# Optimization experiments

Hardware: AMD Instinct MI355X
Metric: run time of the kernel (lower is better)

The kernel has to match this reference:

```python
import jax, jax.numpy as jnp
from jax import lax
import numpy as np

B, T, IN, H, OUT = 1024, 512, 64, 128, 2
BN_EPS = 1e-5


def _gru_layer(x, w_ih, w_hh, b_ih, b_hh):
    # x: [B, T, F]; w_ih: [3H, F]; w_hh: [3H, H]; gate order = (r, z, n) as in PyTorch
    Bb = x.shape[0]
    Hh = w_hh.shape[1]
    xg = jnp.einsum('btf,gf->btg', x, w_ih) + b_ih  # precompute input gates [B, T, 3H]

    def step(h, xg_t):
        hg = h @ w_hh.T + b_hh                       # [B, 3H]
        xr, xz, xn = jnp.split(xg_t, 3, axis=-1)
        hr, hz, hn = jnp.split(hg, 3, axis=-1)
        r = jax.nn.sigmoid(xr + hr)
        z = jax.nn.sigmoid(xz + hz)
        n = jnp.tanh(xn + r * hn)
        h_new = (1.0 - z) * n + z * h
        return h_new, h_new

    h0 = jnp.zeros((Bb, Hh), dtype=x.dtype)
    _, ys = lax.scan(step, h0, jnp.swapaxes(xg, 0, 1))  # scan over time
    return jnp.swapaxes(ys, 0, 1)                        # [B, T, H]


def setup_inputs() -> dict:
    key = jax.random.key(0)
    ks = jax.random.split(key, 16)
    s_in = 1.0 / np.sqrt(H)  # PyTorch GRU init scale
    d = {
        'x': jax.random.normal(ks[0], (B, T, IN), dtype=jnp.float32),
        'w_ih0': jax.random.uniform(ks[1], (3 * H, IN), minval=-s_in, maxval=s_in),
        'w_hh0': jax.random.uniform(ks[2], (3 * H, H), minval=-s_in, maxval=s_in),
        'b_ih0': jax.random.uniform(ks[3], (3 * H,), minval=-s_in, maxval=s_in),
        'b_hh0': jax.random.uniform(ks[4], (3 * H,), minval=-s_in, maxval=s_in),
        'w_ih1': jax.random.uniform(ks[5], (3 * H, H), minval=-s_in, maxval=s_in),
        'w_hh1': jax.random.uniform(ks[6], (3 * H, H), minval=-s_in, maxval=s_in),
        'b_ih1': jax.random.uniform(ks[7], (3 * H,), minval=-s_in, maxval=s_in),
        'b_hh1': jax.random.uniform(ks[8], (3 * H,), minval=-s_in, maxval=s_in),
        'fc1_w': jax.random.normal(ks[9], (H // 2, H)) * 0.05,
        'fc1_b': jnp.zeros((H // 2,)),
        'fc2_w': jax.random.normal(ks[10], (OUT, H // 2)) * 0.05,
        'fc2_b': jnp.zeros((OUT,)),
        'bn_gamma': jnp.ones((H // 2,)),
        'bn_beta': jnp.zeros((H // 2,)),
        'bn_mean': jnp.zeros((H // 2,)),
        'bn_var': jnp.ones((H // 2,)),
    }
    return d


def reference(x, w_ih0, w_hh0, b_ih0, b_hh0, w_ih1, w_hh1, b_ih1, b_hh1,
              fc1_w, fc1_b, fc2_w, fc2_b, bn_gamma, bn_beta, bn_mean, bn_var):
    h1 = _gru_layer(x, w_ih0, w_hh0, b_ih0, b_hh0)   # [B, T, H]
    h2 = _gru_layer(h1, w_ih1, w_hh1, b_ih1, b_hh1)  # [B, T, H]
    out = h2[:, -1, :]                                # last timestep [B, H]
    # dropout = identity (eval mode)
    out = jax.nn.relu(out @ fc1_w.T + fc1_b)          # [B, H/2]
    out = (out - bn_mean) * jax.lax.rsqrt(bn_var + BN_EPS) * bn_gamma + bn_beta
    out = out @ fc2_w.T + fc2_b                       # [B, 2]
    return out
```

## Files before the change

### kernel.cpp

```cpp
#include <hip/hip_runtime.h>
#include <hip/hip_bf16.h>

namespace {

typedef _Float16 h16;
typedef _Float16 f16x8 __attribute__((ext_vector_type(8)));
typedef _Float16 f16x4 __attribute__((ext_vector_type(4)));
typedef _Float16 f16x2 __attribute__((ext_vector_type(2)));
typedef float    f32x4 __attribute__((ext_vector_type(4)));

constexpr int T_SEQ = 512;
constexpr int B_SZ  = 1024;
constexpr int H_DIM = 128;
constexpr int ROWS  = 16;
constexpr int NT    = 512;

template <int INDIM, typename InT, bool STORE_ALL>
__global__ __launch_bounds__(NT, 1)
void gru_mfma(const InT* __restrict__ in,
              const float* __restrict__ w_ih,
              const float* __restrict__ w_hh,
              const float* __restrict__ b_ih,
              const float* __restrict__ b_hh,
              h16*  __restrict__ h1out,
              float* __restrict__ h2out)
{
  constexpr int KSH  = H_DIM / 32;
  constexpr int KSX  = INDIM / 32;
  constexpr int KTOT = H_DIM + INDIM;
  constexpr int ROWP = KTOT + 8;

  __shared__ __align__(16) h16 hx[2][ROWS][ROWP];

  const int tid = threadIdx.x;
  const int wv  = tid >> 6;
  const int ln  = tid & 63;
  const int q   = ln >> 4;
  const int lr  = ln & 15;
  const int r0  = blockIdx.x * ROWS;
  const int j0  = wv * 16 + q * 4;

  f16x8 wA[3][KSH];
  f16x8 wB[3][KSX];
  #pragma unroll
  for (int p = 0; p < 3; ++p) {
    const int g = p * H_DIM + wv * 16 + lr;
    #pragma unroll
    for (int ks = 0; ks < KSH; ++ks) {
      const float* pw = w_hh + (size_t)g * H_DIM + ks * 32 + q * 8;
      const float4 v0 = *(const float4*)(pw);
      const float4 v1 = *(const float4*)(pw + 4);
      f16x8 f;
      f[0]=(h16)v0.x; f[1]=(h16)v0.y; f[2]=(h16)v0.z; f[3]=(h16)v0.w;
      f[4]=(h16)v1.x; f[5]=(h16)v1.y; f[6]=(h16)v1.z; f[7]=(h16)v1.w;
      wA[p][ks] = f;
    }
    #pragma unroll
    for (int ks = 0; ks < KSX; ++ks) {
      const float* pw = w_ih + (size_t)g * INDIM + ks * 32 + q * 8;
      const float4 v0 = *(const float4*)(pw);
      const float4 v1 = *(const float4*)(pw + 4);
      f16x8 f;
      f[0]=(h16)v0.x; f[1]=(h16)v0.y; f[2]=(h16)v0.z; f[3]=(h16)v0.w;
      f[4]=(h16)v1.x; f[5]=(h16)v1.y; f[6]=(h16)v1.z; f[7]=(h16)v1.w;
      wB[p][ks] = f;
    }
  }

  f32x4 bR, bZ, bNx, bNh;
  {
    const float4 ir = *(const float4*)&b_ih[j0];
    const float4 hr = *(const float4*)&b_hh[j0];
    const float4 iz = *(const float4*)&b_ih[H_DIM + j0];
    const float4 hz = *(const float4*)&b_hh[H_DIM + j0];
    const float4 in_ = *(const float4*)&b_ih[2 * H_DIM + j0];
    const float4 hn = *(const float4*)&b_hh[2 * H_DIM + j0];
    bR[0]=ir.x+hr.x; bR[1]=ir.y+hr.y; bR[2]=ir.z+hr.z; bR[3]=ir.w+hr.w;
    bZ[0]=iz.x+hz.x; bZ[1]=iz.y+hz.y; bZ[2]=iz.z+hz.z; bZ[3]=iz.w+hz.w;
    bNx[0]=in_.x; bNx[1]=in_.y; bNx[2]=in_.z; bNx[3]=in_.w;
    bNh[0]=hn.x;  bNh[1]=hn.y;  bNh[2]=hn.z;  bNh[3]=hn.w;
  }

  const int sr = tid >> 5;
  const int si = tid & 31;

  auto load_stage = [&](int t, f16x4& dst) {
    if constexpr (INDIM == 64) {
      const float2 v = *(const float2*)(in + ((size_t)(r0 + sr) * T_SEQ + t) * 64 + si * 2);
      dst[0] = (h16)v.x; dst[1] = (h16)v.y;
    } else {
      dst = *(const f16x4*)(in + ((size_t)t * B_SZ + (r0 + sr)) * 128 + si * 4);
    }
  };
  auto write_stage = [&](int buf, const f16x4& s) {
    if constexpr (INDIM == 64) {
      f16x2 v; v[0] = s[0]; v[1] = s[1];
      *(f16x2*)&hx[buf][sr][H_DIM + si * 2] = v;
    } else {
      *(f16x4*)&hx[buf][sr][H_DIM + si * 4] = s;
    }
  };

  {
    const int zr = tid >> 5, zc = (tid & 31) * 4;
    f16x4 z; z[0] = z[1] = z[2] = z[3] = (h16)0.f;
    *(f16x4*)&hx[0][zr][zc] = z;
  }
  f16x4 s0; load_stage(0, s0); write_stage(0, s0);
  f16x4 sA; load_stage(1, sA);
  f16x4 sB;
  f16x4 h_old; h_old[0] = h_old[1] = h_old[2] = h_old[3] = (h16)0.f;
  __syncthreads();

  auto step = [&](int t, int cur, f16x4& s_use, f16x4& s_load) {
    f16x8 bh[KSH], bx[KSX];
    #pragma unroll
    for (int ks = 0; ks < KSH; ++ks)
      bh[ks] = *(const f16x8*)&hx[cur][lr][ks * 32 + q * 8];
    #pragma unroll
    for (int ks = 0; ks < KSX; ++ks)
      bx[ks] = *(const f16x8*)&hx[cur][lr][H_DIM + ks * 32 + q * 8];

    load_stage((t + 2 < T_SEQ) ? t + 2 : T_SEQ - 1, s_load);

    f32x4 aR = bR, aZ = bZ, aNh = bNh, aNx = bNx;
    #pragma unroll
    for (int ks = 0; ks < KSH; ++ks) {
      aR  = __builtin_amdgcn_mfma_f32_16x16x32_f16(wA[0][ks], bh[ks], aR, 0, 0, 0);
      aZ  = __builtin_amdgcn_mfma_f32_16x16x32_f16(wA[1][ks], bh[ks], aZ, 0, 0, 0);
      aNh = __builtin_amdgcn_mfma_f32_16x16x32_f16(wA[2][ks], bh[ks], aNh, 0, 0, 0);
    }
    #pragma unroll
    for (int ks = 0; ks < KSX; ++ks) {
      aR  = __builtin_amdgcn_mfma_f32_16x16x32_f16(wB[0][ks], bx[ks], aR, 0, 0, 0);
      aZ  = __builtin_amdgcn_mfma_f32_16x16x32_f16(wB[1][ks], bx[ks], aZ, 0, 0, 0);
      aNx = __builtin_amdgcn_mfma_f32_16x16x32_f16(wB[2][ks], bx[ks], aNx, 0, 0, 0);
    }

    f16x4 nv4;
    float hnv[4];
    #pragma unroll
    for (int i = 0; i < 4; ++i) {
      const float rg = __builtin_amdgcn_rcpf(1.f + __expf(-aR[i]));
      const float zg = __builtin_amdgcn_rcpf(1.f + __expf(-aZ[i]));
      const float na = aNx[i] + rg * aNh[i];
      const float e2 = __expf(2.f * na);
      const float ng = 1.f - 2.f * __builtin_amdgcn_rcpf(e2 + 1.f);
      const float ho = (float)h_old[i];
      const float hn = ng + zg * (ho - ng);
      hnv[i] = hn;
      nv4[i] = (h16)hn;
    }
    h_old = nv4;

    *(f16x4*)&hx[cur ^ 1][lr][j0] = nv4;
    write_stage(cur ^ 1, s_use);
    if constexpr (STORE_ALL) {
      *(f16x4*)&h1out[((size_t)t * B_SZ + r0 + lr) * H_DIM + j0] = nv4;
    } else {
      if (t == T_SEQ - 1)
        *(float4*)&h2out[(size_t)(r0 + lr) * H_DIM + j0] =
            make_float4(hnv[0], hnv[1], hnv[2], hnv[3]);
    }
    __syncthreads();
  };

  #pragma unroll 1
  for (int t = 0; t < T_SEQ; t += 2) {
    step(t,     0, sA, sB);
    step(t + 1, 1, sB, sA);
  }
}

__global__ __launch_bounds__(64)
void head_kernel(const float* __restrict__ h2,
                 const float* __restrict__ fc1_w,
                 const float* __restrict__ fc1_b,
                 const float* __restrict__ fc2_w,
                 const float* __restrict__ fc2_b,
                 const float* __restrict__ gamma,
                 const float* __restrict__ beta,
                 const float* __restrict__ mean,
                 const float* __restrict__ var,
                 float* __restrict__ out)
{
  const int row = blockIdx.x;
  const int j   = threadIdx.x;
  __shared__ __align__(16) float hrow[H_DIM];
  __shared__ __align__(16) float act[64];

  hrow[j]      = h2[(size_t)row * H_DIM + j];
  hrow[64 + j] = h2[(size_t)row * H_DIM + 64 + j];
  __syncthreads();

  float s = fc1_b[j];
  const float4* wr = reinterpret_cast<const float4*>(fc1_w + (size_t)j * H_DIM);
  #pragma unroll
  for (int k4 = 0; k4 < H_DIM / 4; ++k4) {
    const float4 w = wr[k4];
    const float4 h = reinterpret_cast<const float4*>(hrow)[k4];
    s += w.x * h.x + w.y * h.y + w.z * h.z + w.w * h.w;
  }
  s = fmaxf(s, 0.f);
  s = (s - mean[j]) * rsqrtf(var[j] + 1e-5f) * gamma[j] + beta[j];
  act[j] = s;
  __syncthreads();

  if (j < 2) {
    float o = fc2_b[j];
    #pragma unroll
    for (int k = 0; k < 64; ++k) o += fc2_w[(size_t)j * 64 + k] * act[k];
    out[(size_t)row * 2 + j] = o;
  }
}

}

extern "C" void kernel_launch(void* const* d_in, const int* in_sizes, int n_in,
                              void* d_out, int out_size, void* d_ws, size_t ws_size,
                              hipStream_t stream) {
  const float* x     = (const float*)d_in[0];
  const float* w_ih0 = (const float*)d_in[1];
  const float* w_hh0 = (const float*)d_in[2];
  const float* b_ih0 = (const float*)d_in[3];
  const float* b_hh0 = (const float*)d_in[4];
  const float* w_ih1 = (const float*)d_in[5];
  const float* w_hh1 = (const float*)d_in[6];
  const float* b_ih1 = (const float*)d_in[7];
  const float* b_hh1 = (const float*)d_in[8];
  const float* fc1_w = (const float*)d_in[9];
  const float* fc1_b = (const float*)d_in[10];
  const float* fc2_w = (const float*)d_in[11];
  const float* fc2_b = (const float*)d_in[12];
  const float* gamma = (const float*)d_in[13];
  const float* beta  = (const float*)d_in[14];
  const float* mean  = (const float*)d_in[15];
  const float* var   = (const float*)d_in[16];
  float* out = (float*)d_out;

  char* ws = (char*)d_ws;
  const size_t h2_bytes = (size_t)B_SZ * H_DIM * sizeof(float);
  const size_t h1_bytes = (size_t)T_SEQ * B_SZ * H_DIM * sizeof(h16);
  if (ws_size < h2_bytes + h1_bytes) return;

  float* h2 = (float*)ws;
  h16*   h1 = (h16*)(ws + h2_bytes);

  gru_mfma<64, float, true><<<dim3(B_SZ / ROWS), dim3(NT), 0, stream>>>(
      x, w_ih0, w_hh0, b_ih0, b_hh0, h1, nullptr);
  gru_mfma<128, h16, false><<<dim3(B_SZ / ROWS), dim3(NT), 0, stream>>>(
      h1, w_ih1, w_hh1, b_ih1, b_hh1, nullptr, h2);
  head_kernel<<<dim3(B_SZ), dim3(64), 0, stream>>>(
      h2, fc1_w, fc1_b, fc2_w, fc2_b, gamma, beta, mean, var, out);
}
```

Baseline: 748.1 us.

## Halve GRU block to four waves with two hidden tiles per wave

The GRU recurrence kernel now runs 256 threads per block instead of 512. Each wave computes two 16-wide hidden tiles, so it holds twice the weights in registers and issues twice the MFMAs per step. Input staging is widened to match, and the LDS row padding changes from 8 to 4 halves. The aim is to make the per-step __syncthreads cheaper and give each wave more independent MFMA chains to overlap, at the cost of higher register pressure and a possible change in LDS bank conflicts.

```diff
diff --git a/kernel.cpp b/kernel.cpp
--- a/kernel.cpp
+++ b/kernel.cpp
@@ -6,14 +6,18 @@
 typedef _Float16 h16;
 typedef _Float16 f16x8 __attribute__((ext_vector_type(8)));
 typedef _Float16 f16x4 __attribute__((ext_vector_type(4)));
-typedef _Float16 f16x2 __attribute__((ext_vector_type(2)));
 typedef float    f32x4 __attribute__((ext_vector_type(4)));
 
 constexpr int T_SEQ = 512;
 constexpr int B_SZ  = 1024;
 constexpr int H_DIM = 128;
 constexpr int ROWS  = 16;
-constexpr int NT    = 512;
+constexpr int NT    = 256;
+constexpr int TILES = 2;
+
+template <int INDIM> struct StageT;
+template <> struct StageT<64>  { using type = f16x4; };
+template <> struct StageT<128> { using type = f16x8; };
 
 template <int INDIM, typename InT, bool STORE_ALL>
 __global__ __launch_bounds__(NT, 1)
@@ -28,7 +32,9 @@
   constexpr int KSH  = H_DIM / 32;
   constexpr int KSX  = INDIM / 32;
   constexpr int KTOT = H_DIM + INDIM;
-  constexpr int ROWP = KTOT + 8;
+  constexpr int ROWP = KTOT + 4;
+
+  using Stage = typename StageT<INDIM>::type;
 
   __shared__ __align__(16) h16 hx[2][ROWS][ROWP];
 
@@ -38,81 +44,85 @@
   const int q   = ln >> 4;
   const int lr  = ln & 15;
   const int r0  = blockIdx.x * ROWS;
-  const int j0  = wv * 16 + q * 4;
-
-  f16x8 wA[3][KSH];
-  f16x8 wB[3][KSX];
+  int j0t[TILES];
+  #pragma unroll
+  for (int ti = 0; ti < TILES; ++ti) j0t[ti] = wv * 32 + ti * 16 + q * 4;
+
+  f16x8 wA[3][TILES][KSH];
+  f16x8 wB[3][TILES][KSX];
   #pragma unroll
   for (int p = 0; p < 3; ++p) {
-    const int g = p * H_DIM + wv * 16 + lr;
-    #pragma unroll
-    for (int ks = 0; ks < KSH; ++ks) {
-      const float* pw = w_hh + (size_t)g * H_DIM + ks * 32 + q * 8;
-      const float4 v0 = *(const float4*)(pw);
-      const float4 v1 = *(const float4*)(pw + 4);
-      f16x8 f;
-      f[0]=(h16)v0.x; f[1]=(h16)v0.y; f[2]=(h16)v0.z; f[3]=(h16)v0.w;
-      f[4]=(h16)v1.x; f[5]=(h16)v1.y; f[6]=(h16)v1.z; f[7]=(h16)v1.w;
-      wA[p][ks] = f;
-    }
-    #pragma unroll
-    for (int ks = 0; ks < KSX; ++ks) {
-      const float* pw = w_ih + (size_t)g * INDIM + ks * 32 + q * 8;
-      const float4 v0 = *(const float4*)(pw);
-      const float4 v1 = *(const float4*)(pw + 4);
-      f16x8 f;
-      f[0]=(h16)v0.x; f[1]=(h16)v0.y; f[2]=(h16)v0.z; f[3]=(h16)v0.w;
-      f[4]=(h16)v1.x; f[5]=(h16)v1.y; f[6]=(h16)v1.z; f[7]=(h16)v1.w;
-      wB[p][ks] = f;
-    }
-  }
-
-  f32x4 bR, bZ, bNx, bNh;
+    #pragma unroll
+    for (int ti = 0; ti < TILES; ++ti) {
+      const int g = p * H_DIM + wv * 32 + ti * 16 + lr;
+      #pragma unroll
+      for (int ks = 0; ks < KSH; ++ks) {
+        const float* pw = w_hh + (size_t)g * H_DIM + ks * 32 + q * 8;
+        const float4 v0 = *(const float4*)(pw);
+        const float4 v1 = *(const float4*)(pw + 4);
+        f16x8 f;
+        f[0]=(h16)v0.x; f[1]=(h16)v0.y; f[2]=(h16)v0.z; f[3]=(h16)v0.w;
+        f[4]=(h16)v1.x; f[5]=(h16)v1.y; f[6]=(h16)v1.z; f[7]=(h16)v1.w;
+        wA[p][ti][ks] = f;
+      }
+      #pragma unroll
+      for (int ks = 0; ks < KSX; ++ks) {
+        const float* pw = w_ih + (size_t)g * INDIM + ks * 32 + q * 8;
+        const float4 v0 = *(const float4*)(pw);
+        const float4 v1 = *(const float4*)(pw + 4);
+        f16x8 f;
+        f[0]=(h16)v0.x; f[1]=(h16)v0.y; f[2]=(h16)v0.z; f[3]=(h16)v0.w;
+        f[4]=(h16)v1.x; f[5]=(h16)v1.y; f[6]=(h16)v1.z; f[7]=(h16)v1.w;
+        wB[p][ti][ks] = f;
+      }
+    }
+  }
+
+  f32x4 bR[TILES], bZ[TILES], bNx[TILES], bNh[TILES];
+  #pragma unroll
+  for (int ti = 0; ti < TILES; ++ti) {
+    const int j0 = j0t[ti];
+    const float4 ir  = *(const float4*)&b_ih[j0];
+    const float4 hr  = *(const float4*)&b_hh[j0];
+    const float4 iz  = *(const float4*)&b_ih[H_DIM + j0];
+    const float4 hz  = *(const float4*)&b_hh[H_DIM + j0];
+    const float4 in_ = *(const float4*)&b_ih[2 * H_DIM + j0];
+    const float4 hn  = *(const float4*)&b_hh[2 * H_DIM + j0];
+    bR[ti][0]=ir.x+hr.x; bR[ti][1]=ir.y+hr.y; bR[ti][2]=ir.z+hr.z; bR[ti][3]=ir.w+hr.w;
+    bZ[ti][0]=iz.x+hz.x; bZ[ti][1]=iz.y+hz.y; bZ[ti][2]=iz.z+hz.z; bZ[ti][3]=iz.w+hz.w;
+    bNx[ti][0]=in_.x; bNx[ti][1]=in_.y; bNx[ti][2]=in_.z; bNx[ti][3]=in_.w;
+    bNh[ti][0]=hn.x;  bNh[ti][1]=hn.y;  bNh[ti][2]=hn.z;  bNh[ti][3]=hn.w;
+  }
+
+  const int sr = tid >> 4;
+  const int si = tid & 15;
+
+  auto load_stage = [&](int t, Stage& dst) {
+    if constexpr (INDIM == 64) {
+      const float4 v = *(const float4*)(in + ((size_t)(r0 + sr) * T_SEQ + t) * 64 + si * 4);
+      dst[0] = (h16)v.x; dst[1] = (h16)v.y; dst[2] = (h16)v.z; dst[3] = (h16)v.w;
+    } else {
+      dst = *(const Stage*)(in + ((size_t)t * B_SZ + (r0 + sr)) * 128 + si * 8);
+    }
+  };
+  auto write_stage = [&](int buf, const Stage& s) {
+    if constexpr (INDIM == 64) *(f16x4*)&hx[buf][sr][H_DIM + si * 4] = s;
+    else                       *(f16x8*)&hx[buf][sr][H_DIM + si * 8] = s;
+  };
+
   {
-    const float4 ir = *(const float4*)&b_ih[j0];
-    const float4 hr = *(const float4*)&b_hh[j0];
-    const float4 iz = *(const float4*)&b_ih[H_DIM + j0];
-    const float4 hz = *(const float4*)&b_hh[H_DIM + j0];
-    const float4 in_ = *(const float4*)&b_ih[2 * H_DIM + j0];
-    const float4 hn = *(const float4*)&b_hh[2 * H_DIM + j0];
-    bR[0]=ir.x+hr.x; bR[1]=ir.y+hr.y; bR[2]=ir.z+hr.z; bR[3]=ir.w+hr.w;
-    bZ[0]=iz.x+hz.x; bZ[1]=iz.y+hz.y; bZ[2]=iz.z+hz.z; bZ[3]=iz.w+hz.w;
-    bNx[0]=in_.x; bNx[1]=in_.y; bNx[2]=in_.z; bNx[3]=in_.w;
-    bNh[0]=hn.x;  bNh[1]=hn.y;  bNh[2]=hn.z;  bNh[3]=hn.w;
-  }
-
-  const int sr = tid >> 5;
-  const int si = tid & 31;
-
-  auto load_stage = [&](int t, f16x4& dst) {
-    if constexpr (INDIM == 64) {
-      const float2 v = *(const float2*)(in + ((size_t)(r0 + sr) * T_SEQ + t) * 64 + si * 2);
-      dst[0] = (h16)v.x; dst[1] = (h16)v.y;
-    } else {
-      dst = *(const f16x4*)(in + ((size_t)t * B_SZ + (r0 + sr)) * 128 + si * 4);
-    }
-  };
-  auto write_stage = [&](int buf, const f16x4& s) {
-    if constexpr (INDIM == 64) {
-      f16x2 v; v[0] = s[0]; v[1] = s[1];
-      *(f16x2*)&hx[buf][sr][H_DIM + si * 2] = v;
-    } else {
-      *(f16x4*)&hx[buf][sr][H_DIM + si * 4] = s;
-    }
-  };
-
-  {
-    const int zr = tid >> 5, zc = (tid & 31) * 4;
-    f16x4 z; z[0] = z[1] = z[2] = z[3] = (h16)0.f;
-    *(f16x4*)&hx[0][zr][zc] = z;
-  }
-  f16x4 s0; load_stage(0, s0); write_stage(0, s0);
-  f16x4 sA; load_stage(1, sA);
-  f16x4 sB;
-  f16x4 h_old; h_old[0] = h_old[1] = h_old[2] = h_old[3] = (h16)0.f;
+    f16x8 z; z[0]=z[1]=z[2]=z[3]=z[4]=z[5]=z[6]=z[7] = (h16)0.f;
+    *(f16x8*)&hx[0][tid >> 4][(tid & 15) * 8] = z;
+  }
+  Stage s0; load_stage(0, s0); write_stage(0, s0);
+  Stage sA; load_stage(1, sA);
+  Stage sB;
+  f16x4 h_old[TILES];
+  #pragma unroll
+  for (int ti = 0; ti < TILES; ++ti) { h_old[ti][0]=h_old[ti][1]=h_old[ti][2]=h_old[ti][3]=(h16)0.f; }
   __syncthreads();
 
-  auto step = [&](int t, int cur, f16x4& s_use, f16x4& s_load) {
+  auto step = [&](int t, int cur, Stage& s_use, Stage& s_load) {
     f16x8 bh[KSH], bx[KSX];
     #pragma unroll
     for (int ks = 0; ks < KSH; ++ks)
@@ -123,45 +133,56 @@
 
     load_stage((t + 2 < T_SEQ) ? t + 2 : T_SEQ - 1, s_load);
 
-    f32x4 aR = bR, aZ = bZ, aNh = bNh, aNx = bNx;
+    f32x4 aR[TILES], aZ[TILES], aNh[TILES], aNx[TILES];
+    #pragma unroll
+    for (int ti = 0; ti < TILES; ++ti) { aR[ti]=bR[ti]; aZ[ti]=bZ[ti]; aNh[ti]=bNh[ti]; aNx[ti]=bNx[ti]; }
     #pragma unroll
     for (int ks = 0; ks < KSH; ++ks) {
-      aR  = __builtin_amdgcn_mfma_f32_16x16x32_f16(wA[0][ks], bh[ks], aR, 0, 0, 0);
-      aZ  = __builtin_amdgcn_mfma_f32_16x16x32_f16(wA[1][ks], bh[ks], aZ, 0, 0, 0);
-      aNh = __builtin_amdgcn_mfma_f32_16x16x32_f16(wA[2][ks], bh[ks], aNh, 0, 0, 0);
+      #pragma unroll
+      for (int ti = 0; ti < TILES; ++ti) {
+        aR[ti]  = __builtin_amdgcn_mfma_f32_16x16x32_f16(wA[0][ti][ks], bh[ks], aR[ti], 0, 0, 0);
+        aZ[ti]  = __builtin_amdgcn_mfma_f32_16x16x32_f16(wA[1][ti][ks], bh[ks], aZ[ti], 0, 0, 0);
+        aNh[ti] = __builtin_amdgcn_mfma_f32_16x16x32_f16(wA[2][ti][ks], bh[ks], aNh[ti], 0, 0, 0);
+      }
     }
     #pragma unroll
     for (int ks = 0; ks < KSX; ++ks) {
-      aR  = __builtin_amdgcn_mfma_f32_16x16x32_f16(wB[0][ks], bx[ks], aR, 0, 0, 0);
-      aZ  = __builtin_amdgcn_mfma_f32_16x16x32_f16(wB[1][ks], bx[ks], aZ, 0, 0, 0);
-      aNx = __builtin_amdgcn_mfma_f32_16x16x32_f16(wB[2][ks], bx[ks], aNx, 0, 0, 0);
-    }
-
-    f16x4 nv4;
-    float hnv[4];
-    #pragma unroll
-    for (int i = 0; i < 4; ++i) {
-      const float rg = __builtin_amdgcn_rcpf(1.f + __expf(-aR[i]));
-      const float zg = __builtin_amdgcn_rcpf(1.f + __expf(-aZ[i]));
-      const float na = aNx[i] + rg * aNh[i];
-      const float e2 = __expf(2.f * na);
-      const float ng = 1.f - 2.f * __builtin_amdgcn_rcpf(e2 + 1.f);
-      const float ho = (float)h_old[i];
-      const float hn = ng + zg * (ho - ng);
-      hnv[i] = hn;
-      nv4[i] = (h16)hn;
-    }
-    h_old = nv4;
-
-    *(f16x4*)&hx[cur ^ 1][lr][j0] = nv4;
+      #pragma unroll
+      for (int ti = 0; ti < TILES; ++ti) {
+        aR[ti]  = __builtin_amdgcn_mfma_f32_16x16x32_f16(wB[0][ti][ks], bx[ks], aR[ti], 0, 0, 0);
+        aZ[ti]  = __builtin_amdgcn_mfma_f32_16x16x32_f16(wB[1][ti][ks], bx[ks], aZ[ti], 0, 0, 0);
+        aNx[ti] = __builtin_amdgcn_mfma_f32_16x16x32_f16(wB[2][ti][ks], bx[ks], aNx[ti], 0, 0, 0);
+      }
+    }
+
+    #pragma unroll
+    for (int ti = 0; ti < TILES; ++ti) {
+      f16x4 nv4;
+      float hnv[4];
+      #pragma unroll
+      for (int i = 0; i < 4; ++i) {
+        const float rg = __builtin_amdgcn_rcpf(1.f + __expf(-aR[ti][i]));
+        const float zg = __builtin_amdgcn_rcpf(1.f + __expf(-aZ[ti][i]));
+        const float na = aNx[ti][i] + rg * aNh[ti][i];
+        const float e2 = __expf(2.f * na);
+        const float ng = 1.f - 2.f * __builtin_amdgcn_rcpf(e2 + 1.f);
+        const float ho = (float)h_old[ti][i];
+        const float hn = ng + zg * (ho - ng);
+        hnv[i] = hn;
+        nv4[i] = (h16)hn;
+      }
+      h_old[ti] = nv4;
+
+      *(f16x4*)&hx[cur ^ 1][lr][j0t[ti]] = nv4;
+      if constexpr (STORE_ALL) {
+        *(f16x4*)&h1out[((size_t)t * B_SZ + r0 + lr) * H_DIM + j0t[ti]] = nv4;
+      } else {
+        if (t == T_SEQ - 1)
+          *(float4*)&h2out[(size_t)(r0 + lr) * H_DIM + j0t[ti]] =
+              make_float4(hnv[0], hnv[1], hnv[2], hnv[3]);
+      }
+    }
     write_stage(cur ^ 1, s_use);
-    if constexpr (STORE_ALL) {
-      *(f16x4*)&h1out[((size_t)t * B_SZ + r0 + lr) * H_DIM + j0] = nv4;
-    } else {
-      if (t == T_SEQ - 1)
-        *(float4*)&h2out[(size_t)(r0 + lr) * H_DIM + j0] =
-            make_float4(hnv[0], hnv[1], hnv[2], hnv[3]);
-    }
     __syncthreads();
   };
 
```

Result: slower. 1.056 ms (+41.1%).

## Fuse both GRU layers into one wavefronted kernel, dropping h1 round-trip

Applied to the files above, without the earlier changes.

Merges the two GRU layer kernels into one kernel that runs layer 1's step t-1 alongside layer 0's step t within a single barrier interval. Layer 0's output goes straight into layer 1's shared-memory input buffer, so the full T×B×H fp16 h1 tensor is never written to or read back from global memory. Two serial 512-step recurrences become one 513-interval pipeline, which roughly halves the number of sequential barrier-separated steps. In exchange each thread holds both layers' weights in registers (about twice the VGPR pressure) and each step carries more MFMA and LDS work. The grid is still only 64 blocks, so per-step latency stays the limiting factor.

```diff
diff --git a/kernel.cpp b/kernel.cpp
--- a/kernel.cpp
+++ b/kernel.cpp
@@ -14,23 +14,24 @@
 constexpr int H_DIM = 128;
 constexpr int ROWS  = 16;
 constexpr int NT    = 512;
-
-template <int INDIM, typename InT, bool STORE_ALL>
+constexpr int KSH   = 4;
+constexpr int KSX0  = 2;
+constexpr int KSX1  = 4;
+constexpr int ROWP0 = 192 + 8;
+constexpr int ROWP1 = 256 + 8;
+
 __global__ __launch_bounds__(NT, 1)
-void gru_mfma(const InT* __restrict__ in,
-              const float* __restrict__ w_ih,
-              const float* __restrict__ w_hh,
-              const float* __restrict__ b_ih,
-              const float* __restrict__ b_hh,
-              h16*  __restrict__ h1out,
-              float* __restrict__ h2out)
+void gru2(const float* __restrict__ x,
+          const float* __restrict__ w_ih0,
+          const float* __restrict__ w_hh0,
+          const float* __restrict__ b_ih0, const float* __restrict__ b_hh0,
+          const float* __restrict__ w_ih1,
+          const float* __restrict__ w_hh1,
+          const float* __restrict__ b_ih1, const float* __restrict__ b_hh1,
+          float* __restrict__ h2out)
 {
-  constexpr int KSH  = H_DIM / 32;
-  constexpr int KSX  = INDIM / 32;
-  constexpr int KTOT = H_DIM + INDIM;
-  constexpr int ROWP = KTOT + 8;
-
-  __shared__ __align__(16) h16 hx[2][ROWS][ROWP];
+  __shared__ __align__(16) h16 hx0[2][ROWS][ROWP0];
+  __shared__ __align__(16) h16 hx1[2][ROWS][ROWP1];
 
   const int tid = threadIdx.x;
   const int wv  = tid >> 6;
@@ -40,105 +41,77 @@
   const int r0  = blockIdx.x * ROWS;
   const int j0  = wv * 16 + q * 4;
 
-  f16x8 wA[3][KSH];
-  f16x8 wB[3][KSX];
+  auto ldw = [](const float* pw) {
+    const float4 v0 = *(const float4*)(pw);
+    const float4 v1 = *(const float4*)(pw + 4);
+    f16x8 f;
+    f[0]=(h16)v0.x; f[1]=(h16)v0.y; f[2]=(h16)v0.z; f[3]=(h16)v0.w;
+    f[4]=(h16)v1.x; f[5]=(h16)v1.y; f[6]=(h16)v1.z; f[7]=(h16)v1.w;
+    return f;
+  };
+
+  f16x8 wA0[3][KSH], wB0[3][KSX0], wA1[3][KSH], wB1[3][KSX1];
   #pragma unroll
   for (int p = 0; p < 3; ++p) {
     const int g = p * H_DIM + wv * 16 + lr;
     #pragma unroll
     for (int ks = 0; ks < KSH; ++ks) {
-      const float* pw = w_hh + (size_t)g * H_DIM + ks * 32 + q * 8;
-      const float4 v0 = *(const float4*)(pw);
-      const float4 v1 = *(const float4*)(pw + 4);
-      f16x8 f;
-      f[0]=(h16)v0.x; f[1]=(h16)v0.y; f[2]=(h16)v0.z; f[3]=(h16)v0.w;
-      f[4]=(h16)v1.x; f[5]=(h16)v1.y; f[6]=(h16)v1.z; f[7]=(h16)v1.w;
-      wA[p][ks] = f;
-    }
-    #pragma unroll
-    for (int ks = 0; ks < KSX; ++ks) {
-      const float* pw = w_ih + (size_t)g * INDIM + ks * 32 + q * 8;
-      const float4 v0 = *(const float4*)(pw);
-      const float4 v1 = *(const float4*)(pw + 4);
-      f16x8 f;
-      f[0]=(h16)v0.x; f[1]=(h16)v0.y; f[2]=(h16)v0.z; f[3]=(h16)v0.w;
-      f[4]=(h16)v1.x; f[5]=(h16)v1.y; f[6]=(h16)v1.z; f[7]=(h16)v1.w;
-      wB[p][ks] = f;
-    }
-  }
-
-  f32x4 bR, bZ, bNx, bNh;
-  {
-    const float4 ir = *(const float4*)&b_ih[j0];
-    const float4 hr = *(const float4*)&b_hh[j0];
-    const float4 iz = *(const float4*)&b_ih[H_DIM + j0];
-    const float4 hz = *(const float4*)&b_hh[H_DIM + j0];
-    const float4 in_ = *(const float4*)&b_ih[2 * H_DIM + j0];
-    const float4 hn = *(const float4*)&b_hh[2 * H_DIM + j0];
-    bR[0]=ir.x+hr.x; bR[1]=ir.y+hr.y; bR[2]=ir.z+hr.z; bR[3]=ir.w+hr.w;
-    bZ[0]=iz.x+hz.x; bZ[1]=iz.y+hz.y; bZ[2]=iz.z+hz.z; bZ[3]=iz.w+hz.w;
-    bNx[0]=in_.x; bNx[1]=in_.y; bNx[2]=in_.z; bNx[3]=in_.w;
-    bNh[0]=hn.x;  bNh[1]=hn.y;  bNh[2]=hn.z;  bNh[3]=hn.w;
+      wA0[p][ks] = ldw(w_hh0 + (size_t)g * H_DIM + ks * 32 + q * 8);
+      wA1[p][ks] = ldw(w_hh1 + (size_t)g * H_DIM + ks * 32 + q * 8);
+    }
+    #pragma unroll
+    for (int ks = 0; ks < KSX0; ++ks)
+      wB0[p][ks] = ldw(w_ih0 + (size_t)g * 64 + ks * 32 + q * 8);
+    #pragma unroll
+    for (int ks = 0; ks < KSX1; ++ks)
+      wB1[p][ks] = ldw(w_ih1 + (size_t)g * H_DIM + ks * 32 + q * 8);
+  }
+
+  f32x4 bR0, bZ0, bNx0, bNh0, bR1, bZ1, bNx1, bNh1;
+  {
+    auto mkb = [&](const float* bi, const float* bh,
+                   f32x4& bR, f32x4& bZ, f32x4& bNx, f32x4& bNh) {
+      const float4 ir  = *(const float4*)&bi[j0];
+      const float4 hr  = *(const float4*)&bh[j0];
+      const float4 iz  = *(const float4*)&bi[H_DIM + j0];
+      const float4 hz  = *(const float4*)&bh[H_DIM + j0];
+      const float4 in_ = *(const float4*)&bi[2 * H_DIM + j0];
+      const float4 hn  = *(const float4*)&bh[2 * H_DIM + j0];
+      bR[0]=ir.x+hr.x; bR[1]=ir.y+hr.y; bR[2]=ir.z+hr.z; bR[3]=ir.w+hr.w;
+      bZ[0]=iz.x+hz.x; bZ[1]=iz.y+hz.y; bZ[2]=iz.z+hz.z; bZ[3]=iz.w+hz.w;
+      bNx[0]=in_.x; bNx[1]=in_.y; bNx[2]=in_.z; bNx[3]=in_.w;
+      bNh[0]=hn.x;  bNh[1]=hn.y;  bNh[2]=hn.z;  bNh[3]=hn.w;
+    };
+    mkb(b_ih0, b_hh0, bR0, bZ0, bNx0, bNh0);
+    mkb(b_ih1, b_hh1, bR1, bZ1, bNx1, bNh1);
   }
 
   const int sr = tid >> 5;
   const int si = tid & 31;
 
-  auto load_stage = [&](int t, f16x4& dst) {
-    if constexpr (INDIM == 64) {
-      const float2 v = *(const float2*)(in + ((size_t)(r0 + sr) * T_SEQ + t) * 64 + si * 2);
-      dst[0] = (h16)v.x; dst[1] = (h16)v.y;
-    } else {
-      dst = *(const f16x4*)(in + ((size_t)t * B_SZ + (r0 + sr)) * 128 + si * 4);
-    }
-  };
-  auto write_stage = [&](int buf, const f16x4& s) {
-    if constexpr (INDIM == 64) {
-      f16x2 v; v[0] = s[0]; v[1] = s[1];
-      *(f16x2*)&hx[buf][sr][H_DIM + si * 2] = v;
-    } else {
-      *(f16x4*)&hx[buf][sr][H_DIM + si * 4] = s;
-    }
-  };
-
-  {
-    const int zr = tid >> 5, zc = (tid & 31) * 4;
-    f16x4 z; z[0] = z[1] = z[2] = z[3] = (h16)0.f;
-    *(f16x4*)&hx[0][zr][zc] = z;
-  }
-  f16x4 s0; load_stage(0, s0); write_stage(0, s0);
-  f16x4 sA; load_stage(1, sA);
-  f16x4 sB;
-  f16x4 h_old; h_old[0] = h_old[1] = h_old[2] = h_old[3] = (h16)0.f;
-  __syncthreads();
-
-  auto step = [&](int t, int cur, f16x4& s_use, f16x4& s_load) {
-    f16x8 bh[KSH], bx[KSX];
-    #pragma unroll
-    for (int ks = 0; ks < KSH; ++ks)
-      bh[ks] = *(const f16x8*)&hx[cur][lr][ks * 32 + q * 8];
-    #pragma unroll
-    for (int ks = 0; ks < KSX; ++ks)
-      bx[ks] = *(const f16x8*)&hx[cur][lr][H_DIM + ks * 32 + q * 8];
-
-    load_stage((t + 2 < T_SEQ) ? t + 2 : T_SEQ - 1, s_load);
-
-    f32x4 aR = bR, aZ = bZ, aNh = bNh, aNx = bNx;
-    #pragma unroll
-    for (int ks = 0; ks < KSH; ++ks) {
-      aR  = __builtin_amdgcn_mfma_f32_16x16x32_f16(wA[0][ks], bh[ks], aR, 0, 0, 0);
-      aZ  = __builtin_amdgcn_mfma_f32_16x16x32_f16(wA[1][ks], bh[ks], aZ, 0, 0, 0);
-      aNh = __builtin_amdgcn_mfma_f32_16x16x32_f16(wA[2][ks], bh[ks], aNh, 0, 0, 0);
-    }
-    #pragma unroll
-    for (int ks = 0; ks < KSX; ++ks) {
-      aR  = __builtin_amdgcn_mfma_f32_16x16x32_f16(wB[0][ks], bx[ks], aR, 0, 0, 0);
-      aZ  = __builtin_amdgcn_mfma_f32_16x16x32_f16(wB[1][ks], bx[ks], aZ, 0, 0, 0);
-      aNx = __builtin_amdgcn_mfma_f32_16x16x32_f16(wB[2][ks], bx[ks], aNx, 0, 0, 0);
-    }
-
+  {
+    f16x4 z; z[0]=z[1]=z[2]=z[3] = (h16)0.f;
+    *(f16x4*)&hx0[0][tid >> 5][(tid & 31) * 4] = z;
+    *(f16x4*)&hx1[1][tid >> 5][(tid & 31) * 4] = z;
+  }
+  {
+    const float2 v = *(const float2*)(x + ((size_t)(r0 + sr) * T_SEQ + 0) * 64 + si * 2);
+    f16x2 s0; s0[0] = (h16)v.x; s0[1] = (h16)v.y;
+    *(f16x2*)&hx0[0][sr][H_DIM + si * 2] = s0;
+  }
+  f16x2 sA, sB;
+  {
+    const float2 v = *(const float2*)(x + ((size_t)(r0 + sr) * T_SEQ + 1) * 64 + si * 2);
+    sA[0] = (h16)v.x; sA[1] = (h16)v.y;
+  }
+  f16x4 h_old0, h_old1;
+  h_old0[0]=h_old0[1]=h_old0[2]=h_old0[3] = (h16)0.f;
+  h_old1 = h_old0;
+  __syncthreads();
+
+  auto gates = [&](const f32x4& aR, const f32x4& aZ, const f32x4& aNx, const f32x4& aNh,
+                   f16x4& h_old, float* hnv) -> f16x4 {
     f16x4 nv4;
-    float hnv[4];
     #pragma unroll
     for (int i = 0; i < 4; ++i) {
       const float rg = __builtin_amdgcn_rcpf(1.f + __expf(-aR[i]));
@@ -152,36 +125,100 @@
       nv4[i] = (h16)hn;
     }
     h_old = nv4;
-
-    *(f16x4*)&hx[cur ^ 1][lr][j0] = nv4;
-    write_stage(cur ^ 1, s_use);
-    if constexpr (STORE_ALL) {
-      *(f16x4*)&h1out[((size_t)t * B_SZ + r0 + lr) * H_DIM + j0] = nv4;
-    } else {
-      if (t == T_SEQ - 1)
-        *(float4*)&h2out[(size_t)(r0 + lr) * H_DIM + j0] =
-            make_float4(hnv[0], hnv[1], hnv[2], hnv[3]);
-    }
+    return nv4;
+  };
+
+  auto l0_step = [&](int g, int cur, f16x2& s_use, f16x2& s_load) {
+    f16x8 bh[KSH], bx[KSX0];
+    #pragma unroll
+    for (int ks = 0; ks < KSH; ++ks)
+      bh[ks] = *(const f16x8*)&hx0[cur][lr][ks * 32 + q * 8];
+    #pragma unroll
+    for (int ks = 0; ks < KSX0; ++ks)
+      bx[ks] = *(const f16x8*)&hx0[cur][lr][H_DIM + ks * 32 + q * 8];
+
+    {
+      const int tt = (g + 2 < T_SEQ) ? g + 2 : T_SEQ - 1;
+      const float2 v = *(const float2*)(x + ((size_t)(r0 + sr) * T_SEQ + tt) * 64 + si * 2);
+      s_load[0] = (h16)v.x; s_load[1] = (h16)v.y;
+    }
+
+    f32x4 aR = bR0, aZ = bZ0, aNh = bNh0, aNx = bNx0;
+    #pragma unroll
+    for (int ks = 0; ks < KSH; ++ks) {
+      aR  = __builtin_amdgcn_mfma_f32_16x16x32_f16(wA0[0][ks], bh[ks], aR, 0, 0, 0);
+      aZ  = __builtin_amdgcn_mfma_f32_16x16x32_f16(wA0[1][ks], bh[ks], aZ, 0, 0, 0);
+      aNh = __builtin_amdgcn_mfma_f32_16x16x32_f16(wA0[2][ks], bh[ks], aNh, 0, 0, 0);
+    }
+    #pragma unroll
+    for (int ks = 0; ks < KSX0; ++ks) {
+      aR  = __builtin_amdgcn_mfma_f32_16x16x32_f16(wB0[0][ks], bx[ks], aR, 0, 0, 0);
+      aZ  = __builtin_amdgcn_mfma_f32_16x16x32_f16(wB0[1][ks], bx[ks], aZ, 0, 0, 0);
+      aNx = __builtin_amdgcn_mfma_f32_16x16x32_f16(wB0[2][ks], bx[ks], aNx, 0, 0, 0);
+    }
+
+    float hnv[4];
+    const f16x4 nv4 = gates(aR, aZ, aNx, aNh, h_old0, hnv);
+    *(f16x4*)&hx0[cur ^ 1][lr][j0] = nv4;
+    *(f16x4*)&hx1[cur ^ 1][lr][H_DIM + j0] = nv4;
+    *(f16x2*)&hx0[cur ^ 1][sr][H_DIM + si * 2] = s_use;
+  };
+
+  auto l1_step = [&](int cur, bool final_store) {
+    f16x8 bh[KSH], bx[KSX1];
+    #pragma unroll
+    for (int ks = 0; ks < KSH; ++ks)
+      bh[ks] = *(const f16x8*)&hx1[cur][lr][ks * 32 + q * 8];
+    #pragma unroll
+    for (int ks = 0; ks < KSX1; ++ks)
+      bx[ks] = *(const f16x8*)&hx1[cur][lr][H_DIM + ks * 32 + q * 8];
+
+    f32x4 aR = bR1, aZ = bZ1, aNh = bNh1, aNx = bNx1;
+    #pragma unroll
+    for (int ks = 0; ks < KSH; ++ks) {
+      aR  = __builtin_amdgcn_mfma_f32_16x16x32_f16(wA1[0][ks], bh[ks], aR, 0, 0, 0);
+      aZ  = __builtin_amdgcn_mfma_f32_16x16x32_f16(wA1[1][ks], bh[ks], aZ, 0, 0, 0);
+      aNh = __builtin_amdgcn_mfma_f32_16x16x32_f16(wA1[2][ks], bh[ks], aNh, 0, 0, 0);
+    }
+    #pragma unroll
+    for (int ks = 0; ks < KSX1; ++ks) {
+      aR  = __builtin_amdgcn_mfma_f32_16x16x32_f16(wB1[0][ks], bx[ks], aR, 0, 0, 0);
+      aZ  = __builtin_amdgcn_mfma_f32_16x16x32_f16(wB1[1][ks], bx[ks], aZ, 0, 0, 0);
+      aNx = __builtin_amdgcn_mfma_f32_16x16x32_f16(wB1[2][ks], bx[ks], aNx, 0, 0, 0);
+    }
+
+    float hnv[4];
+    const f16x4 nv4 = gates(aR, aZ, aNx, aNh, h_old1, hnv);
+    *(f16x4*)&hx1[cur ^ 1][lr][j0] = nv4;
+    if (final_store)
+      *(float4*)&h2out[(size_t)(r0 + lr) * H_DIM + j0] =
+          make_float4(hnv[0], hnv[1], hnv[2], hnv[3]);
+  };
+
+  l0_step(0, 0, sA, sB);
+  __syncthreads();
+
+  #pragma unroll 1
+  for (int k = 0; k < (T_SEQ - 2) / 2; ++k) {
+    l0_step(2 * k + 1, 1, sB, sA);
+    l1_step(1, false);
     __syncthreads();
-  };
-
-  #pragma unroll 1
-  for (int t = 0; t < T_SEQ; t += 2) {
-    step(t,     0, sA, sB);
-    step(t + 1, 1, sB, sA);
-  }
+    l0_step(2 * k + 2, 0, sA, sB);
+    l1_step(0, false);
+    __syncthreads();
+  }
+  l0_step(T_SEQ - 1, 1, sB, sA);
+  l1_step(1, false);
+  __syncthreads();
+  l1_step(0, true);
 }
 
 __global__ __launch_bounds__(64)
 void head_kernel(const float* __restrict__ h2,
-                 const float* __restrict__ fc1_w,
-                 const float* __restrict__ fc1_b,
-                 const float* __restrict__ fc2_w,
-                 const float* __restrict__ fc2_b,
-                 const float* __restrict__ gamma,
-                 const float* __restrict__ beta,
-                 const float* __restrict__ mean,
-                 const float* __restrict__ var,
+                 const float* __restrict__ fc1_w, const float* __restrict__ fc1_b,
+                 const float* __restrict__ fc2_w, const float* __restrict__ fc2_b,
+                 const float* __restrict__ gamma, const float* __restrict__ beta,
+                 const float* __restrict__ mean,  const float* __restrict__ var,
                  float* __restrict__ out)
 {
   const int row = blockIdx.x;
@@ -238,18 +275,12 @@
   const float* var   = (const float*)d_in[16];
   float* out = (float*)d_out;
 
-  char* ws = (char*)d_ws;
   const size_t h2_bytes = (size_t)B_SZ * H_DIM * sizeof(float);
-  const size_t h1_bytes = (size_t)T_SEQ * B_SZ * H_DIM * sizeof(h16);
-  if (ws_size < h2_bytes + h1_bytes) return;
-
-  float* h2 = (float*)ws;
-  h16*   h1 = (h16*)(ws + h2_bytes);
-
-  gru_mfma<64, float, true><<<dim3(B_SZ / ROWS), dim3(NT), 0, stream>>>(
-      x, w_ih0, w_hh0, b_ih0, b_hh0, h1, nullptr);
-  gru_mfma<128, h16, false><<<dim3(B_SZ / ROWS), dim3(NT), 0, stream>>>(
-      h1, w_ih1, w_hh1, b_ih1, b_hh1, nullptr, h2);
+  if (ws_size < h2_bytes) return;
+  float* h2 = (float*)d_ws;
+
+  gru2<<<dim3(B_SZ / ROWS), dim3(NT), 0, stream>>>(
+      x, w_ih0, w_hh0, b_ih0, b_hh0, w_ih1, w_hh1, b_ih1, b_hh1, h2);
   head_kernel<<<dim3(B_SZ), dim3(64), 0, stream>>>(
       h2, fc1_w, fc1_b, fc2_w, fc2_b, gamma, beta, mean, var, out);
 }
```

After: 702.0 us. 1.07x faster.
